# Kernel optimization log

Measured on AMD Instinct MI355X. Metric: run time of the kernel, lower is better.

## Reference

```python
import jax, jax.numpy as jnp
import numpy as np

B, T, D, H, DFF, E = 4, 1024, 1024, 16, 4096, 8
DH = D // H
EPS = 1e-6


def setup_inputs() -> dict:
    key = jax.random.key(0)
    ks = jax.random.split(key, 16)
    s = 0.02
    return {
        "x": jax.random.normal(ks[0], (B, T, D), jnp.float32),
        "mask": jnp.ones((B, 1, 1, T), jnp.bool_),
        "Wq": jax.random.normal(ks[1], (D, D), jnp.float32) * s,
        "bq": jnp.zeros((D,), jnp.float32),
        "Wk": jax.random.normal(ks[2], (D, D), jnp.float32) * s,
        "bk": jnp.zeros((D,), jnp.float32),
        "Wv": jax.random.normal(ks[3], (D, D), jnp.float32) * s,
        "bv": jnp.zeros((D,), jnp.float32),
        "Wo": jax.random.normal(ks[4], (D, D), jnp.float32) * s,
        "bo": jnp.zeros((D,), jnp.float32),
        "ln1_a": jnp.ones((D,), jnp.float32),
        "ln1_b": jnp.zeros((D,), jnp.float32),
        "ln2_a": jnp.ones((D,), jnp.float32),
        "ln2_b": jnp.zeros((D,), jnp.float32),
        "gW": jax.random.normal(ks[5], (D, E), jnp.float32) * s,
        "gb": jnp.zeros((E,), jnp.float32),
        "W1": jax.random.normal(ks[6], (E, D, DFF), jnp.float32) * s,
        "b1": jnp.zeros((E, DFF), jnp.float32),
        "W2": jax.random.normal(ks[7], (E, DFF, D), jnp.float32) * s,
        "b2": jnp.zeros((E, D), jnp.float32),
    }


def layer_norm(x, a, b):
    # Faithful to source: torch std is unbiased (ddof=1), divides by (std + eps)
    mean = jnp.mean(x, -1, keepdims=True)
    std = jnp.std(x, -1, keepdims=True, ddof=1)
    return a * (x - mean) / (std + EPS) + b


def mha(x, mask, Wq, bq, Wk, bk, Wv, bv, Wo, bo):
    def split(h):
        return h.reshape(B, T, H, DH).transpose(0, 2, 1, 3)  # [B,H,T,DH]
    q = split(x @ Wq + bq)
    k = split(x @ Wk + bk)
    v = split(x @ Wv + bv)
    scores = jnp.einsum("bhqd,bhkd->bhqk", q, k) / jnp.sqrt(jnp.float32(DH))
    scores = jnp.where(mask, scores, jnp.float32(-1e9))
    attn = jax.nn.softmax(scores, axis=-1)
    out = jnp.einsum("bhqk,bhkd->bhqd", attn, v)
    out = out.transpose(0, 2, 1, 3).reshape(B, T, D)
    return out @ Wo + bo


def moe(xf, gW, gb, W1, b1, W2, b2):
    # xf: [N, D] flat tokens; top-1 Switch routing
    gate_probs = jax.nn.softmax(xf @ gW + gb, axis=-1)  # [N, E]
    top1_idx = jnp.argmax(gate_probs, axis=-1)          # [N]
    top1_p = jnp.max(gate_probs, axis=-1)               # [N]
    out = jnp.zeros_like(xf)
    for e in range(E):  # fixed small structural loop over experts
        h = jax.nn.relu(xf @ W1[e] + b1[e])
        oe = h @ W2[e] + b2[e]
        sel = (top1_idx == e).astype(xf.dtype)
        out = out + (sel * top1_p)[:, None] * oe
    counts = jax.nn.one_hot(top1_idx, E, dtype=jnp.float32).sum(0)
    aux_loss = jnp.sum((counts / (B * T)) ** 2) * E
    return out, aux_loss


def reference(x, mask, Wq, bq, Wk, bk, Wv, bv, Wo, bo,
              ln1_a, ln1_b, ln2_a, ln2_b, gW, gb, W1, b1, W2, b2):
    # sublayer[0]: x + attn(norm(x))  (dropout=0, inference)
    x1 = x + mha(layer_norm(x, ln1_a, ln1_b), mask, Wq, bq, Wk, bk, Wv, bv, Wo, bo)
    # MoE applied to x1 directly (source calls feed_forward(x), not on the norm)
    ff_out, aux_loss = moe(x1.reshape(-1, D), gW, gb, W1, b1, W2, b2)
    # sublayer[1] with lambda _: ff_out  -> x1 + ff_out (norm computed but discarded)
    x2 = x1 + ff_out.reshape(B, T, D)
    return x2, aux_loss
```

## Files before the change

### kernel.cpp

```cpp
#include <hip/hip_runtime.h>

#define DEV __device__ __forceinline__

typedef unsigned short u16;
typedef __bf16 bf16x8 __attribute__((ext_vector_type(8)));
typedef float f32x4 __attribute__((ext_vector_type(4)));

static constexpr int Bn = 4, Tn = 1024, Dn = 1024, Hn = 16, DFFn = 4096, En = 8;
static constexpr int Nn = Bn * Tn;
static constexpr int MAXT = 40;
static constexpr int HROWS = 5120;

static constexpr int MT_E = 0, MT_P0 = 40, MCNT = 80, MCUR = 88, MSEG = 96, MPERM = 112;

static constexpr size_t WQKVT_O = 0;
static constexpr size_t WOT_O   = WQKVT_O + 3ull * 1024 * 1024 * 2;
static constexpr size_t W12T_O  = WOT_O + 1ull * 1024 * 1024 * 2;
static constexpr size_t X1F_O   = W12T_O + 8ull * 1024 * 4096 * 2;
static constexpr size_t XN_O    = X1F_O + (size_t)Nn * Dn * 4;
static constexpr size_t Q_O     = XN_O + (size_t)Nn * Dn * 2;
static constexpr size_t K_O     = Q_O + (size_t)Nn * Dn * 2;
static constexpr size_t VT_O    = K_O + (size_t)Nn * Dn * 2;
static constexpr size_t X1B_O   = VT_O + (size_t)Nn * Dn * 2;
static constexpr size_t P3_O    = XN_O;
static constexpr size_t H_O     = X1B_O + (size_t)Nn * Dn * 2;
static constexpr size_t TOPP_O  = H_O + (size_t)HROWS * DFFn * 2;
static constexpr size_t TIDX_O  = TOPP_O + (size_t)Nn * 4;
static constexpr size_t META_O  = TIDX_O + (size_t)Nn * 4;

DEV u16 f2bf(float f) {
  union { float f; unsigned u; } v; v.f = f;
  unsigned r = v.u + 0x7fffu + ((v.u >> 16) & 1u);
  return (u16)(r >> 16);
}

DEV void gload16(const void* g, void* l) {
  __builtin_amdgcn_global_load_lds(
      (__attribute__((address_space(1))) void*)(void*)g,
      (__attribute__((address_space(3))) void*)l, 16, 0, 0);
}

DEV void sdecode64(int o, int& row, int& c) {
  row = o >> 7;
  c = ((o >> 4) & 7) ^ (row & 7);
}

DEV int aswz(int r, int c) { return c ^ (r & 7) ^ (((r >> 3) & 3) << 1); }

__global__ __launch_bounds__(256) void tcast_kernel(
    const float* __restrict__ src, u16* __restrict__ dst,
    int R, int C, long srcBatch, long dstBatch) {
  __shared__ u16 tile[64][65];
  src += (long)blockIdx.z * srcBatch;
  dst += (long)blockIdx.z * dstBatch;
  int r0 = blockIdx.y * 64, c0 = blockIdx.x * 64;
  int tr = threadIdx.x >> 4;
  int tc = (threadIdx.x & 15) * 4;
#pragma unroll
  for (int i = 0; i < 4; i++) {
    int r = tr + i * 16;
    float4 v = *reinterpret_cast<const float4*>(&src[(long)(r0 + r) * C + c0 + tc]);
    tile[r][tc + 0] = f2bf(v.x); tile[r][tc + 1] = f2bf(v.y);
    tile[r][tc + 2] = f2bf(v.z); tile[r][tc + 3] = f2bf(v.w);
  }
  __syncthreads();
#pragma unroll
  for (int i = 0; i < 4; i++) {
    int r = tr + i * 16;
    ushort4 o;
    o.x = tile[tc + 0][r]; o.y = tile[tc + 1][r];
    o.z = tile[tc + 2][r]; o.w = tile[tc + 3][r];
    *reinterpret_cast<ushort4*>(&dst[(long)(c0 + r) * R + r0 + tc]) = o;
  }
}

__global__ __launch_bounds__(256) void ln_kernel(
    const float* __restrict__ x, const float* __restrict__ a,
    const float* __restrict__ b, u16* __restrict__ xn) {
  __shared__ float red[8];
  int row = blockIdx.x, tid = threadIdx.x;
  int lane = tid & 63, w = tid >> 6;
  float4 v = *reinterpret_cast<const float4*>(&x[(size_t)row * 1024 + tid * 4]);
  float s = v.x + v.y + v.z + v.w;
  float sq = v.x * v.x + v.y * v.y + v.z * v.z + v.w * v.w;
#pragma unroll
  for (int sh = 1; sh <= 32; sh <<= 1) { s += __shfl_xor(s, sh); sq += __shfl_xor(sq, sh); }
  if (lane == 0) { red[w] = s; red[4 + w] = sq; }
  __syncthreads();
  s = red[0] + red[1] + red[2] + red[3];
  sq = red[4] + red[5] + red[6] + red[7];
  float mean = s * (1.0f / 1024.0f);
  float var = (sq - s * mean) * (1.0f / 1023.0f);
  float inv = 1.0f / (sqrtf(var) + 1e-6f);
  float4 av = *reinterpret_cast<const float4*>(&a[tid * 4]);
  float4 bv = *reinterpret_cast<const float4*>(&b[tid * 4]);
  ushort4 o;
  o.x = f2bf(av.x * (v.x - mean) * inv + bv.x);
  o.y = f2bf(av.y * (v.y - mean) * inv + bv.y);
  o.z = f2bf(av.z * (v.z - mean) * inv + bv.z);
  o.w = f2bf(av.w * (v.w - mean) * inv + bv.w);
  *reinterpret_cast<ushort4*>(&xn[(size_t)row * 1024 + tid * 4]) = o;
}

template <int MODE, int BM, int NG, int KSPLIT>
__global__ __launch_bounds__(256, 3) void gemm3_k(
    const u16* __restrict__ Ag, const u16* __restrict__ Bg,
    const float* __restrict__ f0, const float* __restrict__ f1,
    const float* __restrict__ f2, const float* __restrict__ xres,
    float* __restrict__ x1f, u16* __restrict__ ob0, u16* __restrict__ ob1,
    u16* __restrict__ ob2, float* __restrict__ pout, const int* __restrict__ meta) {
  constexpr int K = (MODE == 3) ? 4096 : 1024;
  constexpr int KS = K / KSPLIT;
  constexpr int NSUB = KS >> 6;
  constexpr int MT = (MODE <= 1) ? (4096 / BM) : MAXT;
  constexpr int NT = (MODE == 0) ? 24 : (MODE == 2) ? 32 : 8;
  constexpr int WR = BM / 2;
  constexpr int MI = WR / 16;
  constexpr int CA = BM / 32;

  __shared__ u16 As[BM * 64];
  __shared__ u16 Bs[128 * 64];

  const int tid = threadIdx.x, lane = tid & 63, w = tid >> 6;
  const int wm = w >> 1, wn = w & 1;
  const int cL = lane >> 4, rl15 = lane & 15;

  constexpr int NWG = MT * NT * KSPLIT;
  constexpr int q8 = NWG >> 3;
  int b = blockIdx.x;
  int lg = (b & 7) * q8 + (b >> 3);
  constexpr int PERG = KSPLIT * MT * NG;
  int g = lg / PERG, rem = lg - g * PERG;
  int s = rem / (MT * NG); rem -= s * (MT * NG);
  int mt = rem / NG;
  int nt = g * NG + (rem - (rem / NG) * NG);

  int m0 = mt * BM, n0 = nt * 128;
  const int k0 = s * KS;
  const u16* Abase = Ag;
  const u16* Bbase = Bg;
  int e = 0, cnt = 0, seg = 0, pos0 = 0;
  if (MODE >= 2) {
    e = meta[MT_E + mt];
    if (e < 0) return;
    cnt = meta[MCNT + e];
    seg = meta[MSEG + e];
    pos0 = meta[MT_P0 + mt];
    Bbase = Bg + (size_t)e * 4096 * 1024;
    if (MODE == 3) Abase = Ag + (size_t)(seg + pos0) * 4096;
    m0 = 0;
  }

  const u16* gA[CA];
  const u16* gB[4];
#pragma unroll
  for (int j = 0; j < CA; j++) {
    int row, c;
    sdecode64(j * 4096 + tid * 16, row, c);
    if constexpr (MODE == 2) {
      int pos = pos0 + row; if (pos >= cnt) pos = cnt - 1;
      int tok = meta[MPERM + seg + pos];
      gA[j] = Ag + (size_t)tok * 1024 + k0 + c * 8;
    } else {
      gA[j] = Abase + (size_t)(m0 + row) * K + k0 + c * 8;
    }
  }
#pragma unroll
  for (int j = 0; j < 4; j++) {
    int row, c;
    sdecode64(j * 4096 + tid * 16, row, c);
    gB[j] = Bbase + (size_t)(n0 + row) * K + k0 + c * 8;
  }

  auto STAGE = [&](int t) {
#pragma unroll
    for (int j = 0; j < CA; j++)
      gload16(gA[j] + t * 64, &As[j * 2048 + tid * 8]);
#pragma unroll
    for (int j = 0; j < 4; j++)
      gload16(gB[j] + t * 64, &Bs[j * 2048 + tid * 8]);
  };

  f32x4 acc[MI][4] = {};
  const char* Ab = reinterpret_cast<const char*>(&As[0]);
  const char* Bb = reinterpret_cast<const char*>(&Bs[0]);

  STAGE(0);
  for (int t = 0; t < NSUB; t++) {
    asm volatile("s_waitcnt vmcnt(0)" ::: "memory");
    __builtin_amdgcn_s_barrier();
#pragma unroll
    for (int ph = 0; ph < 2; ph++) {
      bf16x8 af[MI], bfr[4];
#pragma unroll
      for (int mi = 0; mi < MI; mi++) {
        int row = wm * WR + mi * 16 + rl15;
        af[mi] = *reinterpret_cast<const bf16x8*>(
            Ab + row * 128 + ((ph * 64 + cL * 16) ^ ((row & 7) << 4)));
      }
#pragma unroll
      for (int ni = 0; ni < 4; ni++) {
        int row = wn * 64 + ni * 16 + rl15;
        bfr[ni] = *reinterpret_cast<const bf16x8*>(
            Bb + row * 128 + ((ph * 64 + cL * 16) ^ ((row & 7) << 4)));
      }
#pragma unroll
      for (int mi = 0; mi < MI; mi++)
#pragma unroll
        for (int ni = 0; ni < 4; ni++)
          acc[mi][ni] = __builtin_amdgcn_mfma_f32_16x16x32_bf16(
              af[mi], bfr[ni], acc[mi][ni], 0, 0, 0);
    }
    __builtin_amdgcn_s_barrier();
    if (t + 1 < NSUB) STAGE(t + 1);
  }

  const int cl = rl15, rl = cL;
  if (MODE == 0) {
    int third = n0 >> 10;
    const float* bias = (third == 0) ? f0 : (third == 1) ? f1 : f2;
    const float qs = (third == 0) ? 0.125f : 1.0f;
#pragma unroll
    for (int ni = 0; ni < 4; ni++) {
      int col = n0 + wn * 64 + ni * 16 + cl;
      int jj = col & 1023;
      float bb_ = bias[jj];
      int hh = jj >> 6, dd = jj & 63;
#pragma unroll
      for (int mi = 0; mi < MI; mi++) {
        int t0 = m0 + wm * WR + mi * 16 + rl * 4;
        int b_ = t0 >> 10, tt = t0 & 1023;
        size_t bh = (size_t)(b_ * Hn + hh);
        if (third == 2) {
          ushort4 o4;
          o4.x = f2bf(acc[mi][ni][0] + bb_); o4.y = f2bf(acc[mi][ni][1] + bb_);
          o4.z = f2bf(acc[mi][ni][2] + bb_); o4.w = f2bf(acc[mi][ni][3] + bb_);
          *reinterpret_cast<ushort4*>(&ob2[(bh * 64 + dd) * 1024 + tt]) = o4;
        } else {
          u16* dst = (third == 0) ? ob0 : ob1;
#pragma unroll
          for (int r = 0; r < 4; r++)
            dst[(bh * 1024 + tt + r) * 64 + dd] = f2bf((acc[mi][ni][r] + bb_) * qs);
        }
      }
    }
  } else if (MODE == 1) {
#pragma unroll
    for (int ni = 0; ni < 4; ni++) {
      int col = n0 + wn * 64 + ni * 16 + cl;
      float bo_ = f0[col];
#pragma unroll
      for (int mi = 0; mi < MI; mi++) {
        int row = m0 + wm * WR + mi * 16 + rl * 4;
#pragma unroll
        for (int r = 0; r < 4; r++) {
          size_t idx = (size_t)(row + r) * 1024 + col;
          float v = acc[mi][ni][r] + bo_ + xres[idx];
          x1f[idx] = v;
          ob0[idx] = f2bf(v);
        }
      }
    }
  } else if (MODE == 2) {
#pragma unroll
    for (int ni = 0; ni < 4; ni++) {
      int col = n0 + wn * 64 + ni * 16 + cl;
      float b1_ = f0[(size_t)e * 4096 + col];
#pragma unroll
      for (int mi = 0; mi < MI; mi++) {
        int pos = pos0 + wm * WR + mi * 16 + rl * 4;
#pragma unroll
        for (int r = 0; r < 4; r++) {
          float v = acc[mi][ni][r] + b1_;
          v = v > 0.0f ? v : 0.0f;
          ob0[(size_t)(seg + pos + r) * 4096 + col] = f2bf(v);
        }
      }
    }
  } else {
#pragma unroll
    for (int ni = 0; ni < 4; ni++) {
      int col = n0 + wn * 64 + ni * 16 + cl;
#pragma unroll
      for (int mi = 0; mi < MI; mi++) {
        int pos = pos0 + wm * WR + mi * 16 + rl * 4;
#pragma unroll
        for (int r = 0; r < 4; r++)
          pout[((size_t)s * HROWS + seg + pos + r) * 1024 + col] = acc[mi][ni][r];
      }
    }
  }
}

__global__ __launch_bounds__(256) void reduce3_kernel(
    const float* __restrict__ P3, const float* __restrict__ x1f,
    const float* __restrict__ topp, const float* __restrict__ b2,
    const int* __restrict__ meta, float* __restrict__ out) {
  int bidx = blockIdx.x;
  int tile = bidx >> 7, rowin = bidx & 127;
  int e = meta[MT_E + tile];
  if (e < 0) return;
  int cnt = meta[MCNT + e], seg = meta[MSEG + e];
  int pos = meta[MT_P0 + tile] + rowin;
  if (pos >= cnt) return;
  int tok = meta[MPERM + seg + pos];
  size_t prow = (size_t)(seg + pos) * 1024;
  float p = topp[tok];
  int c = threadIdx.x * 4;
  float4 a0 = *reinterpret_cast<const float4*>(&P3[prow + c]);
  float4 a1 = *reinterpret_cast<const float4*>(&P3[(size_t)HROWS * 1024 + prow + c]);
  float4 xr = *reinterpret_cast<const float4*>(&x1f[(size_t)tok * 1024 + c]);
  float4 bb = *reinterpret_cast<const float4*>(&b2[e * 1024 + c]);
  float4 o;
  o.x = xr.x + p * (a0.x + a1.x + bb.x);
  o.y = xr.y + p * (a0.y + a1.y + bb.y);
  o.z = xr.z + p * (a0.z + a1.z + bb.z);
  o.w = xr.w + p * (a0.w + a1.w + bb.w);
  *reinterpret_cast<float4*>(&out[(size_t)tok * 1024 + c]) = o;
}

__global__ __launch_bounds__(256, 4) void attn_kernel(
    const u16* __restrict__ q, const u16* __restrict__ k,
    const u16* __restrict__ vt, u16* __restrict__ attn) {
  __shared__ u16 Ks[2][64 * 64];
  __shared__ u16 Vs[2][64 * 64];
  const int tid = threadIdx.x, lane = tid & 63, w = tid >> 6;
  const int g = lane >> 4, l15 = lane & 15;

  int bb = blockIdx.x;
  int lg = (bb & 7) * 128 + (bb >> 3);
  const int bh = lg >> 4;
  const int qt = lg & 15;
  const size_t qkbase = (size_t)bh * Tn * 64;
  const size_t vtbase = (size_t)bh * 64 * Tn;
  const int qrow0 = qt * 64 + w * 16;

  bf16x8 qf[2];
  {
    const u16* qp = q + qkbase + (size_t)(qrow0 + l15) * 64 + g * 8;
    qf[0] = *reinterpret_cast<const bf16x8*>(qp);
    qf[1] = *reinterpret_cast<const bf16x8*>(qp + 32);
  }

  const u16* gk[2];
  const u16* gv[2];
#pragma unroll
  for (int j = 0; j < 2; j++) {
    int sidx = j * 256 + tid;
    int r = sidx >> 3, p = sidx & 7;
    int c = aswz(r, p);
    gk[j] = k + qkbase + (size_t)r * 64 + c * 8;
    gv[j] = vt + vtbase + (size_t)r * Tn + c * 8;
  }

  auto STAGE = [&](int t) {
    int buf = t & 1;
#pragma unroll
    for (int j = 0; j < 2; j++) {
      int sidx = j * 256 + tid;
      gload16(gk[j] + (size_t)t * 4096, &Ks[buf][sidx * 8]);
      gload16(gv[j] + (size_t)t * 64, &Vs[buf][sidx * 8]);
    }
  };

  f32x4 o[4] = {};
  float mrun = -1e30f, lsum = 0.0f;

  STAGE(0);
  for (int t = 0; t < 16; t++) {
    asm volatile("s_waitcnt vmcnt(0)" ::: "memory");
    __builtin_amdgcn_s_barrier();
    if (t + 1 < 16) STAGE(t + 1);

    const char* Kb = reinterpret_cast<const char*>(&Ks[t & 1][0]);
    const char* Vb = reinterpret_cast<const char*>(&Vs[t & 1][0]);

    f32x4 sk[2][2];
#pragma unroll
    for (int kb = 0; kb < 2; kb++)
#pragma unroll
      for (int m = 0; m < 2; m++) {
        f32x4 sa = {};
#pragma unroll
        for (int ph = 0; ph < 2; ph++) {
          int ksel = kb * 32 + (l15 >> 2) * 8 + m * 4 + (lane & 3);
          int pch = aswz(ksel, g + ph * 4);
          bf16x8 kf = *reinterpret_cast<const bf16x8*>(Kb + ksel * 128 + pch * 16);
          sa = __builtin_amdgcn_mfma_f32_16x16x32_bf16(kf, qf[ph], sa, 0, 0, 0);
        }
        sk[kb][m] = sa;
      }

    float mx = -1e30f;
#pragma unroll
    for (int kb = 0; kb < 2; kb++)
#pragma unroll
      for (int m = 0; m < 2; m++)
#pragma unroll
        for (int r = 0; r < 4; r++) mx = fmaxf(mx, sk[kb][m][r]);
    mx = fmaxf(mx, __shfl_xor(mx, 16));
    mx = fmaxf(mx, __shfl_xor(mx, 32));
    float mn = fmaxf(mrun, mx);
    float rsc = __expf(mrun - mn);
    mrun = mn;

    float pv[2][8];
    float ps = 0.0f;
#pragma unroll
    for (int kb = 0; kb < 2; kb++)
#pragma unroll
      for (int m = 0; m < 2; m++)
#pragma unroll
        for (int r = 0; r < 4; r++) {
          float pe = __expf(sk[kb][m][r] - mn);
          pv[kb][m * 4 + r] = pe;
          ps += pe;
        }
    ps += __shfl_xor(ps, 16);
    ps += __shfl_xor(ps, 32);
    lsum = lsum * rsc + ps;
#pragma unroll
    for (int nf = 0; nf < 4; nf++)
#pragma unroll
      for (int r = 0; r < 4; r++) o[nf][r] *= rsc;

    bf16x8 pf[2];
#pragma unroll
    for (int kb = 0; kb < 2; kb++)
#pragma unroll
      for (int j = 0; j < 8; j++) pf[kb][j] = (__bf16)pv[kb][j];

#pragma unroll
    for (int nf = 0; nf < 4; nf++) {
      int d = nf * 16 + l15;
#pragma unroll
      for (int kb = 0; kb < 2; kb++) {
        int pch = aswz(d, g + kb * 4);
        bf16x8 vf = *reinterpret_cast<const bf16x8*>(Vb + d * 128 + pch * 16);
        o[nf] = __builtin_amdgcn_mfma_f32_16x16x32_bf16(vf, pf[kb], o[nf], 0, 0, 0);
      }
    }
  }

  float inv = 1.0f / lsum;
  int b_ = bh >> 4, h_ = bh & 15;
  int tok = qrow0 + l15;
#pragma unroll
  for (int nf = 0; nf < 4; nf++)
#pragma unroll
    for (int r = 0; r < 4; r++) {
      int d = nf * 16 + g * 4 + r;
      attn[((size_t)(b_ * Tn + tok)) * 1024 + h_ * 64 + d] = f2bf(o[nf][r] * inv);
    }
}

__global__ __launch_bounds__(256) void gate_kernel(
    const float* __restrict__ x1f, const float* __restrict__ gW,
    const float* __restrict__ gb, float* __restrict__ topp,
    int* __restrict__ tidx, int* __restrict__ meta) {
  int lane = threadIdx.x & 63;
  int n = blockIdx.x * 4 + (threadIdx.x >> 6);
  float acc[8] = {};
  const float* xr = x1f + (size_t)n * 1024;
  for (int kk = 0; kk < 16; kk++) {
    int kcol = kk * 64 + lane;
    float xv = xr[kcol];
    float4 g0 = *reinterpret_cast<const float4*>(&gW[kcol * 8]);
    float4 g1 = *reinterpret_cast<const float4*>(&gW[kcol * 8 + 4]);
    acc[0] = fmaf(xv, g0.x, acc[0]); acc[1] = fmaf(xv, g0.y, acc[1]);
    acc[2] = fmaf(xv, g0.z, acc[2]); acc[3] = fmaf(xv, g0.w, acc[3]);
    acc[4] = fmaf(xv, g1.x, acc[4]); acc[5] = fmaf(xv, g1.y, acc[5]);
    acc[6] = fmaf(xv, g1.z, acc[6]); acc[7] = fmaf(xv, g1.w, acc[7]);
  }
#pragma unroll
  for (int e2 = 0; e2 < 8; e2++)
#pragma unroll
    for (int sh = 1; sh <= 32; sh <<= 1) acc[e2] += __shfl_xor(acc[e2], sh);
  if (lane == 0) {
    float best = -1e30f; int bi = 0;
#pragma unroll
    for (int e2 = 0; e2 < 8; e2++) {
      float lgt = acc[e2] + gb[e2];
      if (lgt > best) { best = lgt; bi = e2; }
    }
    float den = 0.0f;
#pragma unroll
    for (int e2 = 0; e2 < 8; e2++) den += __expf(acc[e2] + gb[e2] - best);
    topp[n] = 1.0f / den;
    tidx[n] = bi;
    atomicAdd(&meta[MCNT + bi], 1);
  }
}

__global__ void scan_kernel(int* meta, float* aux_out) {
  if (threadIdx.x == 0) {
    int sb = 0, t = 0;
    float aux = 0.0f;
    for (int e2 = 0; e2 < 8; e2++) {
      meta[MSEG + e2] = sb;
      int c = meta[MCNT + e2];
      int ntile = (c + 127) >> 7;
      for (int i = 0; i < ntile; i++) { meta[MT_E + t] = e2; meta[MT_P0 + t] = i * 128; t++; }
      sb += ntile << 7;
      float fr = (float)c * (1.0f / 4096.0f);
      aux += fr * fr;
    }
    for (; t < MAXT; t++) { meta[MT_E + t] = -1; meta[MT_P0 + t] = 0; }
    aux_out[0] = aux * 8.0f;
  }
}

__global__ __launch_bounds__(256) void scatter_kernel(const int* __restrict__ tidx, int* meta) {
  int n = blockIdx.x * 256 + threadIdx.x;
  int e2 = tidx[n];
  int pos = atomicAdd(&meta[MCUR + e2], 1);
  meta[MPERM + meta[MSEG + e2] + pos] = n;
}

extern "C" void kernel_launch(void* const* d_in, const int* in_sizes, int n_in,
                              void* d_out, int out_size, void* d_ws, size_t ws_size,
                              hipStream_t stream) {
  const float* x   = (const float*)d_in[0];
  const float* Wq  = (const float*)d_in[2];
  const float* bq  = (const float*)d_in[3];
  const float* Wk  = (const float*)d_in[4];
  const float* bk  = (const float*)d_in[5];
  const float* Wv  = (const float*)d_in[6];
  const float* bv  = (const float*)d_in[7];
  const float* Wo  = (const float*)d_in[8];
  const float* bo  = (const float*)d_in[9];
  const float* ln1a = (const float*)d_in[10];
  const float* ln1b = (const float*)d_in[11];
  const float* gW  = (const float*)d_in[14];
  const float* gb  = (const float*)d_in[15];
  const float* W1  = (const float*)d_in[16];
  const float* b1  = (const float*)d_in[17];
  const float* W2  = (const float*)d_in[18];
  const float* b2  = (const float*)d_in[19];
  float* out = (float*)d_out;
  char* ws = (char*)d_ws;

  u16* wqkvt = (u16*)(ws + WQKVT_O);
  u16* wot   = (u16*)(ws + WOT_O);
  u16* w12t  = (u16*)(ws + W12T_O);
  u16* xn    = (u16*)(ws + XN_O);
  u16* qb    = (u16*)(ws + Q_O);
  u16* kb    = (u16*)(ws + K_O);
  u16* vtb   = (u16*)(ws + VT_O);
  float* x1f = (float*)(ws + X1F_O);
  u16* x1b   = (u16*)(ws + X1B_O);
  float* p3  = (float*)(ws + P3_O);
  u16* hb    = (u16*)(ws + H_O);
  float* topp = (float*)(ws + TOPP_O);
  int* tidx  = (int*)(ws + TIDX_O);
  int* meta  = (int*)(ws + META_O);

  hipMemsetAsync(meta + MCNT, 0, 16 * sizeof(int), stream);

  tcast_kernel<<<dim3(16, 16, 1), 256, 0, stream>>>(Wq, wqkvt, 1024, 1024, 0, 0);
  tcast_kernel<<<dim3(16, 16, 1), 256, 0, stream>>>(Wk, wqkvt + 1024 * 1024, 1024, 1024, 0, 0);
  tcast_kernel<<<dim3(16, 16, 1), 256, 0, stream>>>(Wv, wqkvt + 2 * 1024 * 1024, 1024, 1024, 0, 0);
  tcast_kernel<<<dim3(16, 16, 1), 256, 0, stream>>>(Wo, wot, 1024, 1024, 0, 0);
  tcast_kernel<<<dim3(64, 16, 8), 256, 0, stream>>>(W1, w12t, 1024, 4096,
                                                    (long)1024 * 4096, (long)4096 * 1024);

  ln_kernel<<<4096, 256, 0, stream>>>(x, ln1a, ln1b, xn);
  gemm3_k<0, 128, 4, 1><<<768, 256, 0, stream>>>(xn, wqkvt, bq, bk, bv, nullptr, nullptr,
                                                 qb, kb, vtb, nullptr, meta);
  attn_kernel<<<1024, 256, 0, stream>>>(qb, kb, vtb, xn);
  gemm3_k<1, 64, 4, 1><<<512, 256, 0, stream>>>(xn, wot, bo, nullptr, nullptr, x, x1f,
                                                x1b, nullptr, nullptr, nullptr, meta);
  gate_kernel<<<1024, 256, 0, stream>>>(x1f, gW, gb, topp, tidx, meta);
  scan_kernel<<<1, 64, 0, stream>>>(meta, out + (size_t)Nn * Dn);
  scatter_kernel<<<16, 256, 0, stream>>>(tidx, meta);
  gemm3_k<2, 128, 4, 1><<<1280, 256, 0, stream>>>(x1b, w12t, b1, nullptr, nullptr, nullptr,
                                                  nullptr, hb, nullptr, nullptr, nullptr, meta);
  tcast_kernel<<<dim3(16, 64, 8), 256, 0, stream>>>(W2, w12t, 4096, 1024,
                                                    (long)4096 * 1024, (long)1024 * 4096);
  gemm3_k<3, 128, 2, 2><<<640, 256, 0, stream>>>(hb, w12t, b2, topp, nullptr, nullptr,
                                                 nullptr, nullptr, nullptr, nullptr, p3, meta);
  reduce3_kernel<<<MAXT * 128, 256, 0, stream>>>(p3, x1f, topp, b2, meta, out);
}
```

Before: 393.3 us.

## Double-buffer LDS tiles in GEMM kernels to overlap global loads with MFMA

Changes the shared GEMM kernel from a single LDS buffer to two, issuing the next k-tile's global-to-LDS loads before computing on the current one. A partial vmcnt wait lets only the previous stage's loads complete before the barrier. The aim is to hide global memory latency behind MFMA work. In exchange LDS use doubles and launch bounds drop to 2 waves per SIMD for the BM=128 variants, which lowers occupancy.

```diff
diff --git a/kernel.cpp b/kernel.cpp
--- a/kernel.cpp
+++ b/kernel.cpp
@@ -38,6 +38,12 @@
   __builtin_amdgcn_global_load_lds(
       (__attribute__((address_space(1))) void*)(void*)g,
       (__attribute__((address_space(3))) void*)l, 16, 0, 0);
+}
+
+template <int N> DEV void waitvm() {
+  if constexpr (N == 0) asm volatile("s_waitcnt vmcnt(0)" ::: "memory");
+  else if constexpr (N == 6) asm volatile("s_waitcnt vmcnt(6)" ::: "memory");
+  else if constexpr (N == 8) asm volatile("s_waitcnt vmcnt(8)" ::: "memory");
 }
 
 DEV void sdecode64(int o, int& row, int& c) {
@@ -103,7 +109,7 @@
 }
 
 template <int MODE, int BM, int NG, int KSPLIT>
-__global__ __launch_bounds__(256, 3) void gemm3_k(
+__global__ __launch_bounds__(256, BM == 64 ? 3 : 2) void gemm4_k(
     const u16* __restrict__ Ag, const u16* __restrict__ Bg,
     const float* __restrict__ f0, const float* __restrict__ f1,
     const float* __restrict__ f2, const float* __restrict__ xres,
@@ -117,9 +123,10 @@
   constexpr int WR = BM / 2;
   constexpr int MI = WR / 16;
   constexpr int CA = BM / 32;
-
-  __shared__ u16 As[BM * 64];
-  __shared__ u16 Bs[128 * 64];
+  constexpr int L = CA + 4;
+
+  __shared__ u16 As[2][BM * 64];
+  __shared__ u16 Bs[2][128 * 64];
 
   const int tid = threadIdx.x, lane = tid & 63, w = tid >> 6;
   const int wm = w >> 1, wn = w & 1;
@@ -173,22 +180,29 @@
   }
 
   auto STAGE = [&](int t) {
+    int bi = t & 1;
 #pragma unroll
     for (int j = 0; j < CA; j++)
-      gload16(gA[j] + t * 64, &As[j * 2048 + tid * 8]);
+      gload16(gA[j] + t * 64, &As[bi][j * 2048 + tid * 8]);
 #pragma unroll
     for (int j = 0; j < 4; j++)
-      gload16(gB[j] + t * 64, &Bs[j * 2048 + tid * 8]);
+      gload16(gB[j] + t * 64, &Bs[bi][j * 2048 + tid * 8]);
   };
 
   f32x4 acc[MI][4] = {};
-  const char* Ab = reinterpret_cast<const char*>(&As[0]);
-  const char* Bb = reinterpret_cast<const char*>(&Bs[0]);
 
   STAGE(0);
   for (int t = 0; t < NSUB; t++) {
-    asm volatile("s_waitcnt vmcnt(0)" ::: "memory");
+    if (t + 1 < NSUB) {
+      STAGE(t + 1);
+      waitvm<L>();
+    } else {
+      waitvm<0>();
+    }
     __builtin_amdgcn_s_barrier();
+    __builtin_amdgcn_sched_barrier(0);
+    const char* Ab = reinterpret_cast<const char*>(&As[t & 1][0]);
+    const char* Bb = reinterpret_cast<const char*>(&Bs[t & 1][0]);
 #pragma unroll
     for (int ph = 0; ph < 2; ph++) {
       bf16x8 af[MI], bfr[4];
@@ -212,7 +226,6 @@
               af[mi], bfr[ni], acc[mi][ni], 0, 0, 0);
     }
     __builtin_amdgcn_s_barrier();
-    if (t + 1 < NSUB) STAGE(t + 1);
   }
 
   const int cl = rl15, rl = cL;
@@ -565,19 +578,19 @@
                                                     (long)1024 * 4096, (long)4096 * 1024);
 
   ln_kernel<<<4096, 256, 0, stream>>>(x, ln1a, ln1b, xn);
-  gemm3_k<0, 128, 4, 1><<<768, 256, 0, stream>>>(xn, wqkvt, bq, bk, bv, nullptr, nullptr,
+  gemm4_k<0, 128, 4, 1><<<768, 256, 0, stream>>>(xn, wqkvt, bq, bk, bv, nullptr, nullptr,
                                                  qb, kb, vtb, nullptr, meta);
   attn_kernel<<<1024, 256, 0, stream>>>(qb, kb, vtb, xn);
-  gemm3_k<1, 64, 4, 1><<<512, 256, 0, stream>>>(xn, wot, bo, nullptr, nullptr, x, x1f,
+  gemm4_k<1, 64, 4, 1><<<512, 256, 0, stream>>>(xn, wot, bo, nullptr, nullptr, x, x1f,
                                                 x1b, nullptr, nullptr, nullptr, meta);
   gate_kernel<<<1024, 256, 0, stream>>>(x1f, gW, gb, topp, tidx, meta);
   scan_kernel<<<1, 64, 0, stream>>>(meta, out + (size_t)Nn * Dn);
   scatter_kernel<<<16, 256, 0, stream>>>(tidx, meta);
-  gemm3_k<2, 128, 4, 1><<<1280, 256, 0, stream>>>(x1b, w12t, b1, nullptr, nullptr, nullptr,
+  gemm4_k<2, 128, 4, 1><<<1280, 256, 0, stream>>>(x1b, w12t, b1, nullptr, nullptr, nullptr,
                                                   nullptr, hb, nullptr, nullptr, nullptr, meta);
   tcast_kernel<<<dim3(16, 64, 8), 256, 0, stream>>>(W2, w12t, 4096, 1024,
                                                     (long)4096 * 1024, (long)1024 * 4096);
-  gemm3_k<3, 128, 2, 2><<<640, 256, 0, stream>>>(hb, w12t, b2, topp, nullptr, nullptr,
+  gemm4_k<3, 128, 2, 2><<<640, 256, 0, stream>>>(hb, w12t, b2, topp, nullptr, nullptr,
                                                  nullptr, nullptr, nullptr, nullptr, p3, meta);
   reduce3_kernel<<<MAXT * 128, 256, 0, stream>>>(p3, x1f, topp, b2, meta, out);
 }
```

Result: slower. 426.2 us (+8.4%).

## Add 256x256 double-buffered GEMM for QKV and expert-up projections, bf16 split-K partials

Applied to the files above, without the earlier changes.

Adds a 512-thread GEMM kernel with 256x256 output tiles and double-buffered LDS staging using explicit vmcnt waits and MFMA priority raising. It replaces the 128-wide-tile kernel for the QKV projection and the expert up-projection (W1). The routing metadata gains a second tile table at 256-row granularity, and the H buffer grows to match. The split-K partials of the down-projection are now stored as bf16 instead of fp32, which halves that traffic but adds rounding error before the final reduction.

```diff
diff --git a/kernel.cpp b/kernel.cpp
--- a/kernel.cpp
+++ b/kernel.cpp
@@ -8,10 +8,13 @@
 
 static constexpr int Bn = 4, Tn = 1024, Dn = 1024, Hn = 16, DFFn = 4096, En = 8;
 static constexpr int Nn = Bn * Tn;
-static constexpr int MAXT = 40;
-static constexpr int HROWS = 5120;
-
-static constexpr int MT_E = 0, MT_P0 = 40, MCNT = 80, MCUR = 88, MSEG = 96, MPERM = 112;
+static constexpr int MAXT2 = 24;
+static constexpr int MAXT1 = 40;
+static constexpr int HROWS = 6144;
+
+static constexpr int MT2_E = 0, MT2_P0 = 24;
+static constexpr int MT1_E = 48, MT1_P0 = 88;
+static constexpr int MCNT = 128, MCUR = 136, MSEG = 144, MPERM = 152;
 
 static constexpr size_t WQKVT_O = 0;
 static constexpr size_t WOT_O   = WQKVT_O + 3ull * 1024 * 1024 * 2;
@@ -33,11 +36,20 @@
   unsigned r = v.u + 0x7fffu + ((v.u >> 16) & 1u);
   return (u16)(r >> 16);
 }
+DEV float bf2f(u16 x) {
+  union { unsigned u; float f; } v; v.u = ((unsigned)x) << 16;
+  return v.f;
+}
 
 DEV void gload16(const void* g, void* l) {
   __builtin_amdgcn_global_load_lds(
       (__attribute__((address_space(1))) void*)(void*)g,
       (__attribute__((address_space(3))) void*)l, 16, 0, 0);
+}
+
+template <int N> DEV void waitvm() {
+  if constexpr (N == 0) asm volatile("s_waitcnt vmcnt(0)" ::: "memory");
+  else if constexpr (N == 8) asm volatile("s_waitcnt vmcnt(8)" ::: "memory");
 }
 
 DEV void sdecode64(int o, int& row, int& c) {
@@ -102,18 +114,176 @@
   *reinterpret_cast<ushort4*>(&xn[(size_t)row * 1024 + tid * 4]) = o;
 }
 
+template <int MODE, int NG>
+__global__ __launch_bounds__(512, 2) void gemm8_k(
+    const u16* __restrict__ Ag, const u16* __restrict__ Bg,
+    const float* __restrict__ f0, const float* __restrict__ f1,
+    const float* __restrict__ f2, u16* __restrict__ ob0, u16* __restrict__ ob1,
+    u16* __restrict__ ob2, const int* __restrict__ meta) {
+  constexpr int NSUB = 16;
+  constexpr int MT = (MODE == 0) ? 16 : MAXT2;
+  constexpr int NT = (MODE == 0) ? 12 : 16;
+
+  __shared__ u16 As[2][256 * 64];
+  __shared__ u16 Bs[2][256 * 64];
+
+  const int tid = threadIdx.x, lane = tid & 63, w = tid >> 6;
+  const int wm = w >> 2, wn = w & 3;
+  const int cL = lane >> 4, rl15 = lane & 15;
+
+  constexpr int NWG = MT * NT;
+  constexpr int q8 = NWG >> 3;
+  int b = blockIdx.x;
+  int lg = (b & 7) * q8 + (b >> 3);
+  constexpr int PERG = MT * NG;
+  int g = lg / PERG, rem = lg - g * PERG;
+  int mt = rem / NG;
+  int nt = g * NG + (rem - (rem / NG) * NG);
+
+  int m0 = mt * 256, n0 = nt * 256;
+  const u16* Bbase = Bg;
+  int e = 0, cnt = 0, seg = 0, pos0 = 0;
+  if constexpr (MODE == 2) {
+    e = meta[MT2_E + mt];
+    if (e < 0) return;
+    cnt = meta[MCNT + e];
+    seg = meta[MSEG + e];
+    pos0 = meta[MT2_P0 + mt];
+    Bbase = Bg + (size_t)e * 4096 * 1024;
+  }
+
+  const u16* gA[4];
+  const u16* gB[4];
+#pragma unroll
+  for (int j = 0; j < 4; j++) {
+    int row, c;
+    sdecode64(j * 8192 + tid * 16, row, c);
+    if constexpr (MODE == 2) {
+      int pos = pos0 + row; if (pos >= cnt) pos = cnt - 1;
+      int tok = meta[MPERM + seg + pos];
+      gA[j] = Ag + (size_t)tok * 1024 + c * 8;
+    } else {
+      gA[j] = Ag + (size_t)(m0 + row) * 1024 + c * 8;
+    }
+    gB[j] = Bbase + (size_t)(n0 + row) * 1024 + c * 8;
+  }
+
+  auto STAGE = [&](int t) {
+    int bi = t & 1;
+#pragma unroll
+    for (int j = 0; j < 4; j++)
+      gload16(gA[j] + t * 64, &As[bi][j * 4096 + tid * 8]);
+#pragma unroll
+    for (int j = 0; j < 4; j++)
+      gload16(gB[j] + t * 64, &Bs[bi][j * 4096 + tid * 8]);
+  };
+
+  f32x4 acc[8][4] = {};
+
+  STAGE(0);
+  STAGE(1);
+  waitvm<8>();
+  __builtin_amdgcn_s_barrier();
+
+  for (int t = 0;; t++) {
+    const char* Ab = reinterpret_cast<const char*>(&As[t & 1][0]);
+    const char* Bb = reinterpret_cast<const char*>(&Bs[t & 1][0]);
+#pragma unroll
+    for (int kh = 0; kh < 2; kh++) {
+      bf16x8 bfr[4];
+#pragma unroll
+      for (int ni = 0; ni < 4; ni++) {
+        int row = wn * 64 + ni * 16 + rl15;
+        bfr[ni] = *reinterpret_cast<const bf16x8*>(
+            Bb + row * 128 + ((kh * 64 + cL * 16) ^ ((row & 7) << 4)));
+      }
+#pragma unroll
+      for (int h = 0; h < 2; h++) {
+        bf16x8 af[4];
+#pragma unroll
+        for (int mi2 = 0; mi2 < 4; mi2++) {
+          int row = wm * 128 + h * 64 + mi2 * 16 + rl15;
+          af[mi2] = *reinterpret_cast<const bf16x8*>(
+              Ab + row * 128 + ((kh * 64 + cL * 16) ^ ((row & 7) << 4)));
+        }
+        __builtin_amdgcn_s_setprio(1);
+#pragma unroll
+        for (int mi2 = 0; mi2 < 4; mi2++)
+#pragma unroll
+          for (int ni = 0; ni < 4; ni++)
+            acc[h * 4 + mi2][ni] = __builtin_amdgcn_mfma_f32_16x16x32_bf16(
+                af[mi2], bfr[ni], acc[h * 4 + mi2][ni], 0, 0, 0);
+        __builtin_amdgcn_s_setprio(0);
+      }
+    }
+    if (t == NSUB - 1) break;
+    asm volatile("s_waitcnt lgkmcnt(0)" ::: "memory");
+    __builtin_amdgcn_sched_barrier(0);
+    __builtin_amdgcn_s_barrier();
+    if (t + 2 < NSUB) { STAGE(t + 2); waitvm<8>(); }
+    else waitvm<0>();
+    __builtin_amdgcn_s_barrier();
+  }
+
+  const int cl = rl15, rl = cL;
+  if constexpr (MODE == 0) {
+    int third = n0 >> 10;
+    const float* bias = (third == 0) ? f0 : (third == 1) ? f1 : f2;
+    const float qs = (third == 0) ? 0.125f : 1.0f;
+#pragma unroll
+    for (int ni = 0; ni < 4; ni++) {
+      int col = n0 + wn * 64 + ni * 16 + cl;
+      int jj = col & 1023;
+      float bb_ = bias[jj];
+      int hh = jj >> 6, dd = jj & 63;
+#pragma unroll
+      for (int mi = 0; mi < 8; mi++) {
+        int t0 = m0 + wm * 128 + mi * 16 + rl * 4;
+        int b_ = t0 >> 10, tt = t0 & 1023;
+        size_t bh = (size_t)(b_ * Hn + hh);
+        if (third == 2) {
+          ushort4 o4;
+          o4.x = f2bf(acc[mi][ni][0] + bb_); o4.y = f2bf(acc[mi][ni][1] + bb_);
+          o4.z = f2bf(acc[mi][ni][2] + bb_); o4.w = f2bf(acc[mi][ni][3] + bb_);
+          *reinterpret_cast<ushort4*>(&ob2[(bh * 64 + dd) * 1024 + tt]) = o4;
+        } else {
+          u16* dst = (third == 0) ? ob0 : ob1;
+#pragma unroll
+          for (int r = 0; r < 4; r++)
+            dst[(bh * 1024 + tt + r) * 64 + dd] = f2bf((acc[mi][ni][r] + bb_) * qs);
+        }
+      }
+    }
+  } else {
+#pragma unroll
+    for (int ni = 0; ni < 4; ni++) {
+      int col = n0 + wn * 64 + ni * 16 + cl;
+      float b1_ = f0[(size_t)e * 4096 + col];
+#pragma unroll
+      for (int mi = 0; mi < 8; mi++) {
+        int pos = pos0 + wm * 128 + mi * 16 + rl * 4;
+#pragma unroll
+        for (int r = 0; r < 4; r++) {
+          float v = acc[mi][ni][r] + b1_;
+          v = v > 0.0f ? v : 0.0f;
+          ob0[(size_t)(seg + pos + r) * 4096 + col] = f2bf(v);
+        }
+      }
+    }
+  }
+}
+
 template <int MODE, int BM, int NG, int KSPLIT>
 __global__ __launch_bounds__(256, 3) void gemm3_k(
     const u16* __restrict__ Ag, const u16* __restrict__ Bg,
-    const float* __restrict__ f0, const float* __restrict__ f1,
-    const float* __restrict__ f2, const float* __restrict__ xres,
-    float* __restrict__ x1f, u16* __restrict__ ob0, u16* __restrict__ ob1,
-    u16* __restrict__ ob2, float* __restrict__ pout, const int* __restrict__ meta) {
+    const float* __restrict__ f0, const float* __restrict__ xres,
+    float* __restrict__ x1f, u16* __restrict__ ob0,
+    u16* __restrict__ pout, const int* __restrict__ meta) {
   constexpr int K = (MODE == 3) ? 4096 : 1024;
   constexpr int KS = K / KSPLIT;
   constexpr int NSUB = KS >> 6;
-  constexpr int MT = (MODE <= 1) ? (4096 / BM) : MAXT;
-  constexpr int NT = (MODE == 0) ? 24 : (MODE == 2) ? 32 : 8;
+  constexpr int MT = (MODE == 1) ? (4096 / BM) : MAXT1;
+  constexpr int NT = 8;
   constexpr int WR = BM / 2;
   constexpr int MI = WR / 16;
   constexpr int CA = BM / 32;
@@ -139,15 +309,14 @@
   const int k0 = s * KS;
   const u16* Abase = Ag;
   const u16* Bbase = Bg;
-  int e = 0, cnt = 0, seg = 0, pos0 = 0;
-  if (MODE >= 2) {
-    e = meta[MT_E + mt];
+  int e = 0, seg = 0, pos0 = 0;
+  if constexpr (MODE == 3) {
+    e = meta[MT1_E + mt];
     if (e < 0) return;
-    cnt = meta[MCNT + e];
     seg = meta[MSEG + e];
-    pos0 = meta[MT_P0 + mt];
+    pos0 = meta[MT1_P0 + mt];
     Bbase = Bg + (size_t)e * 4096 * 1024;
-    if (MODE == 3) Abase = Ag + (size_t)(seg + pos0) * 4096;
+    Abase = Ag + (size_t)(seg + pos0) * 4096;
     m0 = 0;
   }
 
@@ -157,13 +326,7 @@
   for (int j = 0; j < CA; j++) {
     int row, c;
     sdecode64(j * 4096 + tid * 16, row, c);
-    if constexpr (MODE == 2) {
-      int pos = pos0 + row; if (pos >= cnt) pos = cnt - 1;
-      int tok = meta[MPERM + seg + pos];
-      gA[j] = Ag + (size_t)tok * 1024 + k0 + c * 8;
-    } else {
-      gA[j] = Abase + (size_t)(m0 + row) * K + k0 + c * 8;
-    }
+    gA[j] = Abase + (size_t)(m0 + row) * K + k0 + c * 8;
   }
 #pragma unroll
   for (int j = 0; j < 4; j++) {
@@ -216,35 +379,7 @@
   }
 
   const int cl = rl15, rl = cL;
-  if (MODE == 0) {
-    int third = n0 >> 10;
-    const float* bias = (third == 0) ? f0 : (third == 1) ? f1 : f2;
-    const float qs = (third == 0) ? 0.125f : 1.0f;
-#pragma unroll
-    for (int ni = 0; ni < 4; ni++) {
-      int col = n0 + wn * 64 + ni * 16 + cl;
-      int jj = col & 1023;
-      float bb_ = bias[jj];
-      int hh = jj >> 6, dd = jj & 63;
-#pragma unroll
-      for (int mi = 0; mi < MI; mi++) {
-        int t0 = m0 + wm * WR + mi * 16 + rl * 4;
-        int b_ = t0 >> 10, tt = t0 & 1023;
-        size_t bh = (size_t)(b_ * Hn + hh);
-        if (third == 2) {
-          ushort4 o4;
-          o4.x = f2bf(acc[mi][ni][0] + bb_); o4.y = f2bf(acc[mi][ni][1] + bb_);
-          o4.z = f2bf(acc[mi][ni][2] + bb_); o4.w = f2bf(acc[mi][ni][3] + bb_);
-          *reinterpret_cast<ushort4*>(&ob2[(bh * 64 + dd) * 1024 + tt]) = o4;
-        } else {
-          u16* dst = (third == 0) ? ob0 : ob1;
-#pragma unroll
-          for (int r = 0; r < 4; r++)
-            dst[(bh * 1024 + tt + r) * 64 + dd] = f2bf((acc[mi][ni][r] + bb_) * qs);
-        }
-      }
-    }
-  } else if (MODE == 1) {
+  if constexpr (MODE == 1) {
 #pragma unroll
     for (int ni = 0; ni < 4; ni++) {
       int col = n0 + wn * 64 + ni * 16 + cl;
@@ -261,61 +396,45 @@
         }
       }
     }
-  } else if (MODE == 2) {
+  } else {
 #pragma unroll
     for (int ni = 0; ni < 4; ni++) {
       int col = n0 + wn * 64 + ni * 16 + cl;
-      float b1_ = f0[(size_t)e * 4096 + col];
 #pragma unroll
       for (int mi = 0; mi < MI; mi++) {
         int pos = pos0 + wm * WR + mi * 16 + rl * 4;
 #pragma unroll
-        for (int r = 0; r < 4; r++) {
-          float v = acc[mi][ni][r] + b1_;
-          v = v > 0.0f ? v : 0.0f;
-          ob0[(size_t)(seg + pos + r) * 4096 + col] = f2bf(v);
-        }
-      }
-    }
-  } else {
-#pragma unroll
-    for (int ni = 0; ni < 4; ni++) {
-      int col = n0 + wn * 64 + ni * 16 + cl;
-#pragma unroll
-      for (int mi = 0; mi < MI; mi++) {
-        int pos = pos0 + wm * WR + mi * 16 + rl * 4;
-#pragma unroll
         for (int r = 0; r < 4; r++)
-          pout[((size_t)s * HROWS + seg + pos + r) * 1024 + col] = acc[mi][ni][r];
+          pout[((size_t)s * HROWS + seg + pos + r) * 1024 + col] = f2bf(acc[mi][ni][r]);
       }
     }
   }
 }
 
 __global__ __launch_bounds__(256) void reduce3_kernel(
-    const float* __restrict__ P3, const float* __restrict__ x1f,
+    const u16* __restrict__ P3, const float* __restrict__ x1f,
     const float* __restrict__ topp, const float* __restrict__ b2,
     const int* __restrict__ meta, float* __restrict__ out) {
   int bidx = blockIdx.x;
   int tile = bidx >> 7, rowin = bidx & 127;
-  int e = meta[MT_E + tile];
+  int e = meta[MT1_E + tile];
   if (e < 0) return;
   int cnt = meta[MCNT + e], seg = meta[MSEG + e];
-  int pos = meta[MT_P0 + tile] + rowin;
+  int pos = meta[MT1_P0 + tile] + rowin;
   if (pos >= cnt) return;
   int tok = meta[MPERM + seg + pos];
   size_t prow = (size_t)(seg + pos) * 1024;
   float p = topp[tok];
   int c = threadIdx.x * 4;
-  float4 a0 = *reinterpret_cast<const float4*>(&P3[prow + c]);
-  float4 a1 = *reinterpret_cast<const float4*>(&P3[(size_t)HROWS * 1024 + prow + c]);
+  ushort4 u0 = *reinterpret_cast<const ushort4*>(&P3[prow + c]);
+  ushort4 u1 = *reinterpret_cast<const ushort4*>(&P3[(size_t)HROWS * 1024 + prow + c]);
   float4 xr = *reinterpret_cast<const float4*>(&x1f[(size_t)tok * 1024 + c]);
   float4 bb = *reinterpret_cast<const float4*>(&b2[e * 1024 + c]);
   float4 o;
-  o.x = xr.x + p * (a0.x + a1.x + bb.x);
-  o.y = xr.y + p * (a0.y + a1.y + bb.y);
-  o.z = xr.z + p * (a0.z + a1.z + bb.z);
-  o.w = xr.w + p * (a0.w + a1.w + bb.w);
+  o.x = xr.x + p * (bf2f(u0.x) + bf2f(u1.x) + bb.x);
+  o.y = xr.y + p * (bf2f(u0.y) + bf2f(u1.y) + bb.y);
+  o.z = xr.z + p * (bf2f(u0.z) + bf2f(u1.z) + bb.z);
+  o.w = xr.w + p * (bf2f(u0.w) + bf2f(u1.w) + bb.w);
   *reinterpret_cast<float4*>(&out[(size_t)tok * 1024 + c]) = o;
 }
 
@@ -494,18 +613,21 @@
 
 __global__ void scan_kernel(int* meta, float* aux_out) {
   if (threadIdx.x == 0) {
-    int sb = 0, t = 0;
+    int sb = 0, t2 = 0, t1 = 0;
     float aux = 0.0f;
     for (int e2 = 0; e2 < 8; e2++) {
       meta[MSEG + e2] = sb;
       int c = meta[MCNT + e2];
-      int ntile = (c + 127) >> 7;
-      for (int i = 0; i < ntile; i++) { meta[MT_E + t] = e2; meta[MT_P0 + t] = i * 128; t++; }
-      sb += ntile << 7;
+      int n2 = (c + 255) >> 8;
+      for (int i = 0; i < n2; i++) { meta[MT2_E + t2] = e2; meta[MT2_P0 + t2] = i * 256; t2++; }
+      int n1 = (c + 127) >> 7;
+      for (int i = 0; i < n1; i++) { meta[MT1_E + t1] = e2; meta[MT1_P0 + t1] = i * 128; t1++; }
+      sb += n2 << 8;
       float fr = (float)c * (1.0f / 4096.0f);
       aux += fr * fr;
     }
-    for (; t < MAXT; t++) { meta[MT_E + t] = -1; meta[MT_P0 + t] = 0; }
+    for (; t2 < MAXT2; t2++) { meta[MT2_E + t2] = -1; meta[MT2_P0 + t2] = 0; }
+    for (; t1 < MAXT1; t1++) { meta[MT1_E + t1] = -1; meta[MT1_P0 + t1] = 0; }
     aux_out[0] = aux * 8.0f;
   }
 }
@@ -549,7 +671,7 @@
   u16* vtb   = (u16*)(ws + VT_O);
   float* x1f = (float*)(ws + X1F_O);
   u16* x1b   = (u16*)(ws + X1B_O);
-  float* p3  = (float*)(ws + P3_O);
+  u16* p3    = (u16*)(ws + P3_O);
   u16* hb    = (u16*)(ws + H_O);
   float* topp = (float*)(ws + TOPP_O);
   int* tidx  = (int*)(ws + TIDX_O);
@@ -565,19 +687,17 @@
                                                     (long)1024 * 4096, (long)4096 * 1024);
 
   ln_kernel<<<4096, 256, 0, stream>>>(x, ln1a, ln1b, xn);
-  gemm3_k<0, 128, 4, 1><<<768, 256, 0, stream>>>(xn, wqkvt, bq, bk, bv, nullptr, nullptr,
-                                                 qb, kb, vtb, nullptr, meta);
+  gemm8_k<0, 4><<<192, 512, 0, stream>>>(xn, wqkvt, bq, bk, bv, qb, kb, vtb, meta);
   attn_kernel<<<1024, 256, 0, stream>>>(qb, kb, vtb, xn);
-  gemm3_k<1, 64, 4, 1><<<512, 256, 0, stream>>>(xn, wot, bo, nullptr, nullptr, x, x1f,
-                                                x1b, nullptr, nullptr, nullptr, meta);
+  gemm3_k<1, 64, 4, 1><<<512, 256, 0, stream>>>(xn, wot, bo, x, x1f, x1b, nullptr, meta);
   gate_kernel<<<1024, 256, 0, stream>>>(x1f, gW, gb, topp, tidx, meta);
   scan_kernel<<<1, 64, 0, stream>>>(meta, out + (size_t)Nn * Dn);
   scatter_kernel<<<16, 256, 0, stream>>>(tidx, meta);
-  gemm3_k<2, 128, 4, 1><<<1280, 256, 0, stream>>>(x1b, w12t, b1, nullptr, nullptr, nullptr,
-                                                  nullptr, hb, nullptr, nullptr, nullptr, meta);
+  gemm8_k<2, 4><<<384, 512, 0, stream>>>(x1b, w12t, b1, nullptr, nullptr, hb, nullptr,
+                                         nullptr, meta);
   tcast_kernel<<<dim3(16, 64, 8), 256, 0, stream>>>(W2, w12t, 4096, 1024,
                                                     (long)4096 * 1024, (long)1024 * 4096);
-  gemm3_k<3, 128, 2, 2><<<640, 256, 0, stream>>>(hb, w12t, b2, topp, nullptr, nullptr,
-                                                 nullptr, nullptr, nullptr, nullptr, p3, meta);
-  reduce3_kernel<<<MAXT * 128, 256, 0, stream>>>(p3, x1f, topp, b2, meta, out);
-}
+  gemm3_k<3, 128, 2, 2><<<640, 256, 0, stream>>>(hb, w12t, nullptr, nullptr, nullptr,
+                                                 nullptr, p3, meta);
+  reduce3_kernel<<<MAXT1 * 128, 256, 0, stream>>>(p3, x1f, topp, b2, meta, out);
+}
```

After: 422.1 us. +7.3%, slower.
